# Optimization experiments

Hardware: AMD Instinct MI355X
Metric: run time of the kernel (lower is better)

The kernel has to match this reference:

```python
import jax, jax.numpy as jnp
import numpy as np
import math

B, L, DV = 8, 2048, 512
FACTOR = 5
SAMPLE_K = min(FACTOR * int(np.ceil(np.log(L))), L)  # 40
N_TOP = min(FACTOR * int(np.ceil(np.log(L))), L)     # 40


def setup_inputs() -> dict:
    key = jax.random.key(0)
    k1, k2, k3, k4, k5 = jax.random.split(key, 5)
    x = jax.random.normal(k1, (B, L, DV), dtype=jnp.float32)
    Wq = jax.random.normal(k2, (DV, DV), dtype=jnp.float32) * (1.0 / math.sqrt(DV))
    Wk = jax.random.normal(k3, (DV, DV), dtype=jnp.float32) * (1.0 / math.sqrt(DV))
    Wv = jax.random.normal(k4, (DV, DV), dtype=jnp.float32) * (1.0 / math.sqrt(DV))
    index_sample = jax.random.randint(k5, (L, SAMPLE_K), 0, L, dtype=jnp.int32)
    return {"x": x, "Wq": Wq, "Wk": Wk, "Wv": Wv, "index_sample": index_sample}


def reference(x, Wq, Wk, Wv, index_sample):
    # Projections (torch Linear, no bias): y = x @ W.T
    Q = x @ Wq.T  # [B, L, D]
    K = x @ Wk.T  # [B, L, D]
    V = x @ Wv.T  # [B, L, D]
    b, L_Q, D = Q.shape
    L_K = K.shape[1]

    # _prob_QK: sample keys per query, score sparsity measure M
    K_sample = K[:, index_sample, :]                       # [B, L_Q, sample_k, D]
    QK_sample = jnp.einsum('bld,blsd->bls', Q, K_sample)   # [B, L_Q, sample_k]
    M = QK_sample.max(axis=-1) - QK_sample.sum(axis=-1) / L_K  # [B, L_Q]
    _, M_top = jax.lax.top_k(M, N_TOP)                     # [B, n_top]

    Q_reduce = jnp.take_along_axis(Q, M_top[:, :, None], axis=1)  # [B, n_top, D]
    scores = jnp.einsum('bud,bkd->buk', Q_reduce, K)       # [B, n_top, L_K]
    scores = scores * (1.0 / math.sqrt(D))

    # mask_flag=False -> initial context is mean of V broadcast over queries
    attn = jax.nn.softmax(scores, axis=-1)
    context = jnp.broadcast_to(V.mean(axis=1, keepdims=True), (b, L_Q, D))
    upd = attn @ V                                         # [B, n_top, D]
    context = context.at[jnp.arange(b)[:, None], M_top].set(upd)
    return context
```

## Files before the change

kernel.cpp:

```cpp
#include <hip/hip_runtime.h>
#include <hip/hip_bf16.h>
#include <math.h>

#define BATCH 8
#define LSEQ 2048
#define DIM 512
#define SK 40
#define NTOP 40

typedef __attribute__((ext_vector_type(8))) short bf16x8;
typedef __attribute__((ext_vector_type(4))) float f32x4;

__device__ inline void split1(float f, ushort& h, ushort& l) {
    __hip_bfloat16 bh = __float2bfloat16(f);
    float r = f - __bfloat162float(bh);
    __hip_bfloat16 bl = __float2bfloat16(r);
    h = *reinterpret_cast<ushort*>(&bh);
    l = *reinterpret_cast<ushort*>(&bl);
}

__global__ __launch_bounds__(256) void convert_all(
    const float* __restrict__ x,
    const float* __restrict__ w0, const float* __restrict__ w1, const float* __restrict__ w2,
    ushort* __restrict__ xh, ushort* __restrict__ xl,
    ushort* __restrict__ wh, ushort* __restrict__ wl)
{
    const int bx = blockIdx.x;
    const float* src;
    ushort *dh, *dl;
    int i;
    if (bx < 8192) {
        i = (bx * 256 + (int)threadIdx.x) * 4;
        src = x; dh = xh; dl = xl;
    } else {
        const int j = bx - 8192;
        const int z = j >> 8;
        src = (z == 0) ? w0 : (z == 1) ? w1 : w2;
        dh = wh + (size_t)z * DIM * DIM;
        dl = wl + (size_t)z * DIM * DIM;
        i = ((j & 255) * 256 + (int)threadIdx.x) * 4;
    }
    float4 v = *reinterpret_cast<const float4*>(src + i);
    ushort4 h, l;
    split1(v.x, h.x, l.x); split1(v.y, h.y, l.y);
    split1(v.z, h.z, l.z); split1(v.w, h.w, l.w);
    *reinterpret_cast<ushort4*>(dh + i) = h;
    *reinterpret_cast<ushort4*>(dl + i) = l;
}

__device__ inline void load_lds16(const void* g, void* l) {
    __builtin_amdgcn_global_load_lds(
        (const __attribute__((address_space(1))) void*)g,
        (__attribute__((address_space(3))) void*)l, 16, 0, 0);
}

__global__ __launch_bounds__(256) void gemm_mfma(
    const ushort* __restrict__ xh, const ushort* __restrict__ xl,
    const ushort* __restrict__ whAll, const ushort* __restrict__ wlAll,
    float* __restrict__ Q, float* __restrict__ K, float* __restrict__ V)
{
    const ushort* Wh = whAll + (size_t)blockIdx.z * DIM * DIM;
    const ushort* Wl = wlAll + (size_t)blockIdx.z * DIM * DIM;
    float* C = (blockIdx.z == 0) ? Q : (blockIdx.z == 1) ? K : V;

    __shared__ ushort Ah[128 * 32], Al[128 * 32], Bh[128 * 32], Bl[128 * 32];

    const int tid  = threadIdx.x;
    const int lane = tid & 63;
    const int w    = tid >> 6;
    const int row0 = blockIdx.x * 128;
    const int col0 = blockIdx.y * 128;
    const int wr = w >> 1, wc = w & 1;

    const int rA  = w * 16 + (lane >> 2);
    const int sh_ = (lane & 3) ^ ((rA >> 1) & 3);
    const size_t aoff = (size_t)(row0 + rA) * DIM + sh_ * 8;
    const size_t boff = (size_t)(col0 + rA) * DIM + sh_ * 8;

    f32x4 acc[4][4];
    #pragma unroll
    for (int i = 0; i < 4; ++i)
        #pragma unroll
        for (int j = 0; j < 4; ++j)
            acc[i][j] = (f32x4){0.f, 0.f, 0.f, 0.f};

    const int rbA = wr * 64 + (lane & 15);
    const int rbB = wc * 64 + (lane & 15);
    const int kh  = lane >> 4;

    for (int k0 = 0; k0 < DIM; k0 += 32) {
        load_lds16(xh + aoff + k0,            &Ah[w * 512]);
        load_lds16(xh + aoff + 64 * DIM + k0, &Ah[2048 + w * 512]);
        load_lds16(xl + aoff + k0,            &Al[w * 512]);
        load_lds16(xl + aoff + 64 * DIM + k0, &Al[2048 + w * 512]);
        load_lds16(Wh + boff + k0,            &Bh[w * 512]);
        load_lds16(Wh + boff + 64 * DIM + k0, &Bh[2048 + w * 512]);
        load_lds16(Wl + boff + k0,            &Bl[w * 512]);
        load_lds16(Wl + boff + 64 * DIM + k0, &Bl[2048 + w * 512]);
        __syncthreads();

        bf16x8 fah[4], fal[4], fbh[4], fbl[4];
        #pragma unroll
        for (int mf = 0; mf < 4; ++mf) {
            const int r = rbA + mf * 16;
            const int off = r * 32 + (kh ^ ((r >> 1) & 3)) * 8;
            fah[mf] = *reinterpret_cast<const bf16x8*>(&Ah[off]);
            fal[mf] = *reinterpret_cast<const bf16x8*>(&Al[off]);
        }
        #pragma unroll
        for (int nf = 0; nf < 4; ++nf) {
            const int r = rbB + nf * 16;
            const int off = r * 32 + (kh ^ ((r >> 1) & 3)) * 8;
            fbh[nf] = *reinterpret_cast<const bf16x8*>(&Bh[off]);
            fbl[nf] = *reinterpret_cast<const bf16x8*>(&Bl[off]);
        }
        #pragma unroll
        for (int mf = 0; mf < 4; ++mf)
            #pragma unroll
            for (int nf = 0; nf < 4; ++nf) {
                acc[mf][nf] = __builtin_amdgcn_mfma_f32_16x16x32_bf16(fah[mf], fbh[nf], acc[mf][nf], 0, 0, 0);
                acc[mf][nf] = __builtin_amdgcn_mfma_f32_16x16x32_bf16(fal[mf], fbh[nf], acc[mf][nf], 0, 0, 0);
                acc[mf][nf] = __builtin_amdgcn_mfma_f32_16x16x32_bf16(fah[mf], fbl[nf], acc[mf][nf], 0, 0, 0);
            }
        __syncthreads();
    }

    #pragma unroll
    for (int mf = 0; mf < 4; ++mf)
        #pragma unroll
        for (int nf = 0; nf < 4; ++nf) {
            float* cp = C + (size_t)(row0 + wr * 64 + mf * 16 + (lane >> 4) * 4) * DIM
                          + col0 + wc * 64 + nf * 16 + (lane & 15);
            #pragma unroll
            for (int j = 0; j < 4; ++j)
                cp[(size_t)j * DIM] = acc[mf][nf][j];
        }
}

#define BM 64
#define BN 64
#define BKD 32
__global__ __launch_bounds__(256) void gemm_qkv(
    const float* __restrict__ x,
    const float* __restrict__ Wq, const float* __restrict__ Wk, const float* __restrict__ Wv,
    float* __restrict__ Q, float* __restrict__ K, float* __restrict__ V)
{
    const float* W;
    float* C;
    if (blockIdx.z == 0)      { W = Wq; C = Q; }
    else if (blockIdx.z == 1) { W = Wk; C = K; }
    else                      { W = Wv; C = V; }

    __shared__ float As[BKD][BM];
    __shared__ float Bs[BKD][BN];

    const int tid  = threadIdx.x;
    const int row0 = blockIdx.x * BM;
    const int col0 = blockIdx.y * BN;
    const int ty   = tid >> 4;
    const int tx   = tid & 15;
    const int lrow = tid >> 3;
    const int lkq  = tid & 7;

    float acc[4][4] = {};
    for (int k0 = 0; k0 < DIM; k0 += BKD) {
        #pragma unroll
        for (int h = 0; h < 2; ++h) {
            const int arow = lrow + h * 32;
            float4 va = *reinterpret_cast<const float4*>(&x[(size_t)(row0 + arow) * DIM + k0 + lkq * 4]);
            As[lkq * 4 + 0][arow] = va.x; As[lkq * 4 + 1][arow] = va.y;
            As[lkq * 4 + 2][arow] = va.z; As[lkq * 4 + 3][arow] = va.w;
            float4 vb = *reinterpret_cast<const float4*>(&W[(size_t)(col0 + arow) * DIM + k0 + lkq * 4]);
            Bs[lkq * 4 + 0][arow] = vb.x; Bs[lkq * 4 + 1][arow] = vb.y;
            Bs[lkq * 4 + 2][arow] = vb.z; Bs[lkq * 4 + 3][arow] = vb.w;
        }
        __syncthreads();
        #pragma unroll
        for (int kk = 0; kk < BKD; ++kk) {
            float4 a4 = *reinterpret_cast<const float4*>(&As[kk][ty * 4]);
            float4 b4 = *reinterpret_cast<const float4*>(&Bs[kk][tx * 4]);
            float af[4] = {a4.x, a4.y, a4.z, a4.w};
            float bf[4] = {b4.x, b4.y, b4.z, b4.w};
            #pragma unroll
            for (int i = 0; i < 4; ++i)
                #pragma unroll
                for (int j = 0; j < 4; ++j)
                    acc[i][j] += af[i] * bf[j];
        }
        __syncthreads();
    }
    #pragma unroll
    for (int i = 0; i < 4; ++i) {
        float4 o = make_float4(acc[i][0], acc[i][1], acc[i][2], acc[i][3]);
        *reinterpret_cast<float4*>(&C[(size_t)(row0 + ty * 4 + i) * DIM + col0 + tx * 4]) = o;
    }
}

__global__ __launch_bounds__(256) void compute_m(
    const float* __restrict__ Q, const float* __restrict__ K,
    const int* __restrict__ smp, float* __restrict__ M)
{
    const int wv   = threadIdx.x >> 6;
    const int lane = threadIdx.x & 63;
    const int b    = blockIdx.x & 7;
    const int l    = (blockIdx.x >> 3) * 4 + wv;

    const float* qr = Q + ((size_t)b * LSEQ + l) * DIM;
    float4 q0 = *reinterpret_cast<const float4*>(&qr[lane * 8]);
    float4 q1 = *reinterpret_cast<const float4*>(&qr[lane * 8 + 4]);

    const int* sp = smp + l * SK;
    const float* Kb = K + (size_t)b * LSEQ * DIM;

    float mx = -1e30f, sm = 0.0f;
    for (int s = 0; s < SK; s += 4) {
        int4 id = *reinterpret_cast<const int4*>(sp + s);
        const float* r0 = Kb + (size_t)id.x * DIM + lane * 8;
        const float* r1 = Kb + (size_t)id.y * DIM + lane * 8;
        const float* r2 = Kb + (size_t)id.z * DIM + lane * 8;
        const float* r3 = Kb + (size_t)id.w * DIM + lane * 8;
        float4 a0 = *reinterpret_cast<const float4*>(r0);
        float4 a1 = *reinterpret_cast<const float4*>(r0 + 4);
        float4 b0 = *reinterpret_cast<const float4*>(r1);
        float4 b1 = *reinterpret_cast<const float4*>(r1 + 4);
        float4 c0 = *reinterpret_cast<const float4*>(r2);
        float4 c1 = *reinterpret_cast<const float4*>(r2 + 4);
        float4 d0 = *reinterpret_cast<const float4*>(r3);
        float4 d1 = *reinterpret_cast<const float4*>(r3 + 4);

        float p0 = q0.x*a0.x + q0.y*a0.y + q0.z*a0.z + q0.w*a0.w
                 + q1.x*a1.x + q1.y*a1.y + q1.z*a1.z + q1.w*a1.w;
        float p1 = q0.x*b0.x + q0.y*b0.y + q0.z*b0.z + q0.w*b0.w
                 + q1.x*b1.x + q1.y*b1.y + q1.z*b1.z + q1.w*b1.w;
        float p2 = q0.x*c0.x + q0.y*c0.y + q0.z*c0.z + q0.w*c0.w
                 + q1.x*c1.x + q1.y*c1.y + q1.z*c1.z + q1.w*c1.w;
        float p3 = q0.x*d0.x + q0.y*d0.y + q0.z*d0.z + q0.w*d0.w
                 + q1.x*d1.x + q1.y*d1.y + q1.z*d1.z + q1.w*d1.w;
        #pragma unroll
        for (int o = 32; o; o >>= 1) {
            p0 += __shfl_xor(p0, o, 64);
            p1 += __shfl_xor(p1, o, 64);
            p2 += __shfl_xor(p2, o, 64);
            p3 += __shfl_xor(p3, o, 64);
        }
        mx = fmaxf(mx, fmaxf(fmaxf(p0, p1), fmaxf(p2, p3)));
        sm += (p0 + p1) + (p2 + p3);
    }
    if (lane == 0) M[(size_t)b * LSEQ + l] = mx - sm * (1.0f / LSEQ);
}

__global__ __launch_bounds__(1024) void topk_kernel(
    const float* __restrict__ M, int* __restrict__ topidx)
{
    const int b = blockIdx.x;
    __shared__ float vals[LSEQ];
    __shared__ float wv[16];
    __shared__ int   wi[16];
    const int tid  = threadIdx.x;
    const int lane = tid & 63;
    const int wave = tid >> 6;

    vals[tid]        = M[b * LSEQ + tid];
    vals[tid + 1024] = M[b * LSEQ + tid + 1024];
    __syncthreads();

    for (int t = 0; t < NTOP; ++t) {
        float v0 = vals[tid], v1 = vals[tid + 1024];
        float bv; int bi;
        if (v0 >= v1) { bv = v0; bi = tid; } else { bv = v1; bi = tid + 1024; }
        #pragma unroll
        for (int o = 32; o; o >>= 1) {
            float ov = __shfl_xor(bv, o, 64);
            int   oi = __shfl_xor(bi, o, 64);
            if (ov > bv || (ov == bv && oi < bi)) { bv = ov; bi = oi; }
        }
        if (lane == 0) { wv[wave] = bv; wi[wave] = bi; }
        __syncthreads();
        if (wave == 0) {
            float fv = (lane < 16) ? wv[lane] : -1e30f;
            int   fi = (lane < 16) ? wi[lane] : 0x7fffffff;
            #pragma unroll
            for (int o = 8; o; o >>= 1) {
                float ov = __shfl_xor(fv, o, 64);
                int   oi = __shfl_xor(fi, o, 64);
                if (ov > fv || (ov == fv && oi < fi)) { fv = ov; fi = oi; }
            }
            if (lane == 0) {
                topidx[b * NTOP + t] = fi;
                vals[fi] = -1e30f;
            }
        }
        __syncthreads();
    }
}

__global__ __launch_bounds__(256) void vmean_partial(
    const float* __restrict__ V, float* __restrict__ P)
{
    const int b = blockIdx.x & 7, c = blockIdx.x >> 3;
    const int tid = threadIdx.x;
    #pragma unroll
    for (int dd = 0; dd < 2; ++dd) {
        const int d = tid + dd * 256;
        const float* vp = V + ((size_t)b * LSEQ + c * 128) * DIM + d;
        float s = 0.0f;
        for (int r = 0; r < 128; ++r) s += vp[(size_t)r * DIM];
        P[(size_t)(b * 16 + c) * DIM + d] = s;
    }
}

__global__ __launch_bounds__(256) void vmean_reduce(
    const float* __restrict__ P, float* __restrict__ vmean)
{
    const int b = blockIdx.x;
    const int tid = threadIdx.x;
    #pragma unroll
    for (int dd = 0; dd < 2; ++dd) {
        const int d = tid + dd * 256;
        float s = 0.0f;
        #pragma unroll
        for (int c = 0; c < 16; ++c) s += P[(size_t)(b * 16 + c) * DIM + d];
        vmean[b * DIM + d] = s * (1.0f / LSEQ);
    }
}

__global__ __launch_bounds__(256) void fill_out(
    const float4* __restrict__ vmean4, float4* __restrict__ out4)
{
    const int f = blockIdx.x * 256 + threadIdx.x;
    const int d4 = f & 127;
    const int b  = f >> 18;
    out4[f] = vmean4[b * 128 + d4];
}

__global__ __launch_bounds__(256) void scores_kernel(
    const float* __restrict__ Q, const float* __restrict__ K,
    const int* __restrict__ topidx, float* __restrict__ S)
{
    const int b  = blockIdx.x & 7;
    const int lc = blockIdx.x >> 3;
    __shared__ float Qs[40 * 132];
    __shared__ float Ks[64 * 132];
    __shared__ int tix[NTOP];
    const int tid = threadIdx.x;
    const int lt  = tid & 31;
    const int ug  = tid >> 5;
    float acc[2][5] = {};

    if (tid < NTOP) tix[tid] = topidx[b * NTOP + tid];
    __syncthreads();

    for (int d0 = 0; d0 < DIM; d0 += 128) {
        for (int j = tid; j < 1280; j += 256) {
            const int u = j >> 5, d4 = j & 31;
            *reinterpret_cast<float4*>(&Qs[u * 132 + d4 * 4]) =
                *reinterpret_cast<const float4*>(&Q[((size_t)b * LSEQ + tix[u]) * DIM + d0 + d4 * 4]);
        }
        for (int j = tid; j < 2048; j += 256) {
            const int l = j >> 5, d4 = j & 31;
            *reinterpret_cast<float4*>(&Ks[l * 132 + d4 * 4]) =
                *reinterpret_cast<const float4*>(&K[((size_t)b * LSEQ + lc * 64 + l) * DIM + d0 + d4 * 4]);
        }
        __syncthreads();
        for (int d4 = 0; d4 < 32; ++d4) {
            float4 ka = *reinterpret_cast<const float4*>(&Ks[lt * 132 + d4 * 4]);
            float4 kb = *reinterpret_cast<const float4*>(&Ks[(lt + 32) * 132 + d4 * 4]);
            #pragma unroll
            for (int i = 0; i < 5; ++i) {
                float4 q = *reinterpret_cast<const float4*>(&Qs[(ug + i * 8) * 132 + d4 * 4]);
                acc[0][i] += q.x * ka.x + q.y * ka.y + q.z * ka.z + q.w * ka.w;
                acc[1][i] += q.x * kb.x + q.y * kb.y + q.z * kb.z + q.w * kb.w;
            }
        }
        __syncthreads();
    }
    const float scale = 0.044194173824159216f;
    #pragma unroll
    for (int i = 0; i < 5; ++i) {
        const int u = ug + i * 8;
        S[((size_t)(b * NTOP + u)) * LSEQ + lc * 64 + lt]      = acc[0][i] * scale;
        S[((size_t)(b * NTOP + u)) * LSEQ + lc * 64 + lt + 32] = acc[1][i] * scale;
    }
}

__global__ __launch_bounds__(256) void softmax_kernel(
    const float* __restrict__ S, float* __restrict__ Pt)
{
    const int row = blockIdx.x;
    const int b = row / NTOP, u = row % NTOP;
    __shared__ float red[4];
    const int tid  = threadIdx.x;
    const int lane = tid & 63;
    const int wave = tid >> 6;
    const float* sr = S + (size_t)row * LSEQ;

    float v[8];
    float mx = -1e30f;
    #pragma unroll
    for (int j = 0; j < 8; ++j) { v[j] = sr[tid + j * 256]; mx = fmaxf(mx, v[j]); }
    #pragma unroll
    for (int o = 32; o; o >>= 1) mx = fmaxf(mx, __shfl_xor(mx, o, 64));
    if (lane == 0) red[wave] = mx;
    __syncthreads();
    mx = fmaxf(fmaxf(red[0], red[1]), fmaxf(red[2], red[3]));
    __syncthreads();

    float s = 0.0f;
    #pragma unroll
    for (int j = 0; j < 8; ++j) { v[j] = __expf(v[j] - mx); s += v[j]; }
    #pragma unroll
    for (int o = 32; o; o >>= 1) s += __shfl_xor(s, o, 64);
    if (lane == 0) red[wave] = s;
    __syncthreads();
    const float rec = 1.0f / (red[0] + red[1] + red[2] + red[3]);

    #pragma unroll
    for (int j = 0; j < 8; ++j)
        Pt[((size_t)b * LSEQ + tid + j * 256) * NTOP + u] = v[j] * rec;
}

__global__ __launch_bounds__(512) void pv_partial(
    const float* __restrict__ Pt, const float* __restrict__ V, float* __restrict__ Ppart)
{
    const int b  = blockIdx.x & 7;
    const int lc = blockIdx.x >> 3;
    const int d  = threadIdx.x;
    float part[NTOP] = {};
    for (int l = 0; l < 128; ++l) {
        const float v = V[((size_t)b * LSEQ + lc * 128 + l) * DIM + d];
        const float* ps = Pt + ((size_t)b * LSEQ + lc * 128 + l) * NTOP;
        #pragma unroll
        for (int u = 0; u < NTOP; ++u) part[u] = fmaf(ps[u], v, part[u]);
    }
    #pragma unroll
    for (int u = 0; u < NTOP; ++u)
        Ppart[(((size_t)(b * 16 + lc)) * NTOP + u) * DIM + d] = part[u];
}

__global__ __launch_bounds__(512) void pv_reduce(
    const float* __restrict__ Ppart, const int* __restrict__ topidx, float* __restrict__ out)
{
    const int row = blockIdx.x;
    const int b = row / NTOP, u = row % NTOP;
    const int d = threadIdx.x;
    float s = 0.0f;
    #pragma unroll
    for (int lc = 0; lc < 16; ++lc)
        s += Ppart[(((size_t)(b * 16 + lc)) * NTOP + u) * DIM + d];
    out[((size_t)b * LSEQ + topidx[row]) * DIM + d] = s;
}

__global__ __launch_bounds__(256) void att_kernel(
    const float* __restrict__ Q, const float* __restrict__ K, const float* __restrict__ V,
    const int* __restrict__ topidx, float* __restrict__ out)
{
    const int b = blockIdx.x / NTOP;
    const int u = blockIdx.x % NTOP;
    const int l0 = topidx[b * NTOP + u];

    __shared__ float p[LSEQ];
    __shared__ float redm[4];
    __shared__ float reds[4];

    const int tid  = threadIdx.x;
    const int lane = tid & 63;
    const int wave = tid >> 6;

    const float* qr = Q + ((size_t)b * LSEQ + l0) * DIM;
    float4 q0 = *reinterpret_cast<const float4*>(&qr[lane * 8]);
    float4 q1 = *reinterpret_cast<const float4*>(&qr[lane * 8 + 4]);
    const float scale = 0.044194173824159216f;

    for (int it = 0; it < 512; ++it) {
        const int l = wave * 512 + it;
        const float* kr = K + ((size_t)b * LSEQ + l) * DIM;
        float4 k0 = *reinterpret_cast<const float4*>(&kr[lane * 8]);
        float4 k1 = *reinterpret_cast<const float4*>(&kr[lane * 8 + 4]);
        float d = q0.x * k0.x + q0.y * k0.y + q0.z * k0.z + q0.w * k0.w
                + q1.x * k1.x + q1.y * k1.y + q1.z * k1.z + q1.w * k1.w;
        #pragma unroll
        for (int o = 32; o; o >>= 1) d += __shfl_xor(d, o, 64);
        if (lane == 0) p[l] = d * scale;
    }
    __syncthreads();

    float mx = -1e30f;
    for (int i = tid; i < LSEQ; i += 256) mx = fmaxf(mx, p[i]);
    #pragma unroll
    for (int o = 32; o; o >>= 1) mx = fmaxf(mx, __shfl_xor(mx, o, 64));
    if (lane == 0) redm[wave] = mx;
    __syncthreads();
    mx = fmaxf(fmaxf(redm[0], redm[1]), fmaxf(redm[2], redm[3]));

    float s = 0.0f;
    for (int i = tid; i < LSEQ; i += 256) {
        float e = __expf(p[i] - mx);
        s += e;
        p[i] = e;
    }
    #pragma unroll
    for (int o = 32; o; o >>= 1) s += __shfl_xor(s, o, 64);
    if (lane == 0) reds[wave] = s;
    __syncthreads();
    const float rec = 1.0f / (reds[0] + reds[1] + reds[2] + reds[3]);

    float s0 = 0.0f, s1 = 0.0f;
    const float* vp = V + (size_t)b * LSEQ * DIM;
    for (int l = 0; l < LSEQ; ++l) {
        const float w = p[l];
        s0 += w * vp[(size_t)l * DIM + tid];
        s1 += w * vp[(size_t)l * DIM + tid + 256];
    }
    float* orow = out + ((size_t)b * LSEQ + l0) * DIM;
    orow[tid]       = s0 * rec;
    orow[tid + 256] = s1 * rec;
}

extern "C" void kernel_launch(void* const* d_in, const int* in_sizes, int n_in,
                              void* d_out, int out_size, void* d_ws, size_t ws_size,
                              hipStream_t stream)
{
    const float* x   = (const float*)d_in[0];
    const float* Wq  = (const float*)d_in[1];
    const float* Wk  = (const float*)d_in[2];
    const float* Wv  = (const float*)d_in[3];
    const int*   smp = (const int*)d_in[4];
    float* out = (float*)d_out;

    const size_t NQKV = (size_t)BATCH * LSEQ * DIM;
    float* ws = (float*)d_ws;

    float* Q     = ws;
    float* K     = Q + NQKV;
    float* V     = K + NQKV;
    float* Mb    = V + NQKV;
    float* vmP   = Mb + BATCH * LSEQ;
    float* vmean = vmP + BATCH * 16 * DIM;
    float* S     = vmean + BATCH * DIM;
    float* Pt    = S + (size_t)BATCH * NTOP * LSEQ;
    float* Qsel  = Pt + (size_t)BATCH * NTOP * LSEQ;
    float* Ppart = Qsel + (size_t)BATCH * NTOP * DIM;
    int*   topidx = (int*)(Ppart + (size_t)BATCH * 16 * NTOP * DIM);
    ushort* xh = (ushort*)(topidx + BATCH * NTOP);
    ushort* xl = xh + NQKV;
    ushort* wh = xl + NQKV;
    ushort* wl = wh + (size_t)3 * DIM * DIM;
    const size_t need_fast = (size_t)((char*)(wl + (size_t)3 * DIM * DIM) - (char*)d_ws);
    const size_t need_mid  = (size_t)((char*)(topidx + BATCH * NTOP) - (char*)d_ws);

    const bool fast = ws_size >= need_fast;
    const bool mid  = ws_size >= need_mid;

    if (mid) {
        if (fast) {
            convert_all<<<8960, 256, 0, stream>>>(x, Wq, Wk, Wv, xh, xl, wh, wl);
            gemm_mfma<<<dim3(BATCH * LSEQ / 128, DIM / 128, 3), 256, 0, stream>>>(
                xh, xl, wh, wl, Q, K, V);
        } else {
            gemm_qkv<<<dim3(BATCH * LSEQ / BM, DIM / BN, 3), 256, 0, stream>>>(
                x, Wq, Wk, Wv, Q, K, V);
        }
        compute_m<<<4096, 256, 0, stream>>>(Q, K, smp, Mb);
        topk_kernel<<<BATCH, 1024, 0, stream>>>(Mb, topidx);
        vmean_partial<<<BATCH * 16, 256, 0, stream>>>(V, vmP);
        vmean_reduce<<<BATCH, 256, 0, stream>>>(vmP, vmean);
        fill_out<<<(BATCH * LSEQ * DIM / 4) / 256, 256, 0, stream>>>(
            (const float4*)vmean, (float4*)out);
        scores_kernel<<<256, 256, 0, stream>>>(Q, K, topidx, S);
        softmax_kernel<<<BATCH * NTOP, 256, 0, stream>>>(S, Pt);
        pv_partial<<<128, 512, 0, stream>>>(Pt, V, Ppart);
        pv_reduce<<<BATCH * NTOP, 512, 0, stream>>>(Ppart, topidx, out);
    } else {
        float* Qf = ws;
        float* Kf = Qf + NQKV;
        float* Vf = Kf + NQKV;
        float* Mf = Vf + NQKV;
        int*   ti = (int*)(Mf + (size_t)BATCH * LSEQ);
        float* Pf = (float*)(ti + BATCH * NTOP);
        float* vm = Pf + (size_t)BATCH * 16 * DIM;

        gemm_qkv<<<dim3(BATCH * LSEQ / BM, DIM / BN, 3), 256, 0, stream>>>(
            x, Wq, Wk, Wv, Qf, Kf, Vf);
        compute_m<<<4096, 256, 0, stream>>>(Qf, Kf, smp, Mf);
        topk_kernel<<<BATCH, 1024, 0, stream>>>(Mf, ti);
        vmean_partial<<<BATCH * 16, 256, 0, stream>>>(Vf, Pf);
        vmean_reduce<<<BATCH, 256, 0, stream>>>(Pf, vm);
        fill_out<<<(BATCH * LSEQ * DIM / 4) / 256, 256, 0, stream>>>(
            (const float4*)vm, (float4*)out);
        att_kernel<<<BATCH * NTOP, 256, 0, stream>>>(Qf, Kf, Vf, ti, out);
    }
}
```

Baseline: 321.4 us.

## Rewrite QKV split-bf16 GEMM as 256x128 tile, 8-wave, double-buffered pipeline

Replaces the 128x128, 4-wave GEMM with a 256x128, 8-wave kernel. The three hi/lo bf16 product terms are folded into a single 24-step K loop (3 terms x 8 chunks of 64), with double-buffered LDS staging via global_load_lds, explicit vmcnt waits and barriers, and s_setprio around the MFMA bursts. Blocks are remapped with an XCD-aware swizzle so neighbouring tiles share L2, and each block's columns stay within one of Q/K/V. The aim is to overlap global loads with MFMA work and get more reuse per tile, at the cost of more LDS (96 KB) and hand-tuned waitcnt logic that is fragile.

```diff
diff --git a/kernel.cpp b/kernel.cpp
--- a/kernel.cpp
+++ b/kernel.cpp
@@ -54,28 +54,59 @@
         (__attribute__((address_space(3))) void*)l, 16, 0, 0);
 }
 
-__global__ __launch_bounds__(256) void gemm_mfma(
+__global__ __launch_bounds__(512) void gemm8(
     const ushort* __restrict__ xh, const ushort* __restrict__ xl,
     const ushort* __restrict__ whAll, const ushort* __restrict__ wlAll,
     float* __restrict__ Q, float* __restrict__ K, float* __restrict__ V)
 {
-    const ushort* Wh = whAll + (size_t)blockIdx.z * DIM * DIM;
-    const ushort* Wl = wlAll + (size_t)blockIdx.z * DIM * DIM;
-    float* C = (blockIdx.z == 0) ? Q : (blockIdx.z == 1) ? K : V;
-
-    __shared__ ushort Ah[128 * 32], Al[128 * 32], Bh[128 * 32], Bl[128 * 32];
+    __shared__ ushort SA[32768];
+    __shared__ ushort SB[16384];
 
     const int tid  = threadIdx.x;
     const int lane = tid & 63;
     const int w    = tid >> 6;
-    const int row0 = blockIdx.x * 128;
-    const int col0 = blockIdx.y * 128;
-    const int wr = w >> 1, wc = w & 1;
-
-    const int rA  = w * 16 + (lane >> 2);
-    const int sh_ = (lane & 3) ^ ((rA >> 1) & 3);
-    const size_t aoff = (size_t)(row0 + rA) * DIM + sh_ * 8;
-    const size_t boff = (size_t)(col0 + rA) * DIM + sh_ * 8;
+    const int wr   = w >> 1;
+    const int wcn  = w & 1;
+
+    const int wg = ((int)blockIdx.x & 7) * 96 + ((int)blockIdx.x >> 3);
+    const int mb = wg / 12, nb = wg % 12;
+    const int z  = nb >> 2;
+    float* C = (z == 0) ? Q : (z == 1) ? K : V;
+    const int row0  = mb * 256;
+    const int wrow0 = (nb & 3) * 128;
+    const ushort* whb = whAll + (size_t)z * (DIM * DIM);
+    const ushort* wlb = wlAll + (size_t)z * (DIM * DIM);
+
+    int rA[2], dA[2]; size_t sA[2];
+    #pragma unroll
+    for (int i = 0; i < 2; ++i) {
+        const int g = i * 512 + tid;
+        const int row = g >> 2, sl = g & 3;
+        const int ss = sl ^ ((row >> 1) & 3);
+        rA[i] = row;
+        dA[i] = (g & ~63) * 8;
+        sA[i] = (size_t)(row0 + row) * DIM + ss * 8;
+    }
+    int dB; size_t sB;
+    {
+        const int g = tid;
+        const int row = g >> 2, sl = g & 3;
+        const int ss = sl ^ ((row >> 1) & 3);
+        dB = (g & ~63) * 8;
+        sB = (size_t)(wrow0 + row) * DIM + ss * 8;
+    }
+
+    int aoff[4], boff[4];
+    #pragma unroll
+    for (int mf = 0; mf < 4; ++mf) {
+        const int row = wr * 64 + mf * 16 + (lane & 15);
+        aoff[mf] = row * 32 + (((lane >> 4) ^ ((row >> 1) & 3)) * 8);
+    }
+    #pragma unroll
+    for (int nf = 0; nf < 4; ++nf) {
+        const int row = wcn * 64 + nf * 16 + (lane & 15);
+        boff[nf] = row * 32 + (((lane >> 4) ^ ((row >> 1) & 3)) * 8);
+    }
 
     f32x4 acc[4][4];
     #pragma unroll
@@ -84,53 +115,83 @@
         for (int j = 0; j < 4; ++j)
             acc[i][j] = (f32x4){0.f, 0.f, 0.f, 0.f};
 
-    const int rbA = wr * 64 + (lane & 15);
-    const int rbB = wc * 64 + (lane & 15);
-    const int kh  = lane >> 4;
-
-    for (int k0 = 0; k0 < DIM; k0 += 32) {
-        load_lds16(xh + aoff + k0,            &Ah[w * 512]);
-        load_lds16(xh + aoff + 64 * DIM + k0, &Ah[2048 + w * 512]);
-        load_lds16(xl + aoff + k0,            &Al[w * 512]);
-        load_lds16(xl + aoff + 64 * DIM + k0, &Al[2048 + w * 512]);
-        load_lds16(Wh + boff + k0,            &Bh[w * 512]);
-        load_lds16(Wh + boff + 64 * DIM + k0, &Bh[2048 + w * 512]);
-        load_lds16(Wl + boff + k0,            &Bl[w * 512]);
-        load_lds16(Wl + boff + 64 * DIM + k0, &Bl[2048 + w * 512]);
-        __syncthreads();
-
-        bf16x8 fah[4], fal[4], fbh[4], fbl[4];
-        #pragma unroll
-        for (int mf = 0; mf < 4; ++mf) {
-            const int r = rbA + mf * 16;
-            const int off = r * 32 + (kh ^ ((r >> 1) & 3)) * 8;
-            fah[mf] = *reinterpret_cast<const bf16x8*>(&Ah[off]);
-            fal[mf] = *reinterpret_cast<const bf16x8*>(&Al[off]);
-        }
-        #pragma unroll
-        for (int nf = 0; nf < 4; ++nf) {
-            const int r = rbB + nf * 16;
-            const int off = r * 32 + (kh ^ ((r >> 1) & 3)) * 8;
-            fbh[nf] = *reinterpret_cast<const bf16x8*>(&Bh[off]);
-            fbl[nf] = *reinterpret_cast<const bf16x8*>(&Bl[off]);
-        }
-        #pragma unroll
-        for (int mf = 0; mf < 4; ++mf)
-            #pragma unroll
-            for (int nf = 0; nf < 4; ++nf) {
-                acc[mf][nf] = __builtin_amdgcn_mfma_f32_16x16x32_bf16(fah[mf], fbh[nf], acc[mf][nf], 0, 0, 0);
-                acc[mf][nf] = __builtin_amdgcn_mfma_f32_16x16x32_bf16(fal[mf], fbh[nf], acc[mf][nf], 0, 0, 0);
-                acc[mf][nf] = __builtin_amdgcn_mfma_f32_16x16x32_bf16(fah[mf], fbl[nf], acc[mf][nf], 0, 0, 0);
-            }
-        __syncthreads();
-    }
+#define STAGE_CHUNK(t_, ks_, cb_)                                              \
+    {                                                                          \
+        const int tt_ = (t_) >> 3;                                             \
+        const int ksrc_ = (((t_) & 7) << 6) + ((ks_) << 5);                    \
+        const ushort* ap_ = (tt_ == 1) ? xl : xh;                              \
+        const ushort* bp_ = (tt_ == 2) ? wlb : whb;                            \
+        const int ab_ = ((cb_) * 2 + (ks_)) * 8192;                            \
+        const int bb_ = ((cb_) * 2 + (ks_)) * 4096;                            \
+        load_lds16(ap_ + sA[0] + ksrc_, &SA[ab_ + dA[0]]);                     \
+        load_lds16(ap_ + sA[1] + ksrc_, &SA[ab_ + dA[1]]);                     \
+        load_lds16(bp_ + sB + ksrc_,    &SB[bb_ + dB]);                        \
+    }
+
+    STAGE_CHUNK(0, 0, 0)
+    STAGE_CHUNK(0, 1, 0)
+    STAGE_CHUNK(1, 0, 1)
+    asm volatile("s_waitcnt vmcnt(6)" ::: "memory");
+    asm volatile("s_barrier" ::: "memory");
+
+    #pragma unroll 2
+    for (int t = 0; t < 24; ++t) {
+        const int cb = t & 1;
+        {
+            bf16x8 af[4], bf_[4];
+            const int ab = (cb * 2 + 0) * 8192;
+            const int bb = (cb * 2 + 0) * 4096;
+            #pragma unroll
+            for (int mf = 0; mf < 4; ++mf)
+                af[mf] = *reinterpret_cast<const bf16x8*>(&SA[ab + aoff[mf]]);
+            #pragma unroll
+            for (int nf = 0; nf < 4; ++nf)
+                bf_[nf] = *reinterpret_cast<const bf16x8*>(&SB[bb + boff[nf]]);
+            if (t + 1 < 24) STAGE_CHUNK(t + 1, 1, cb ^ 1)
+            asm volatile("s_waitcnt vmcnt(6)" ::: "memory");
+            asm volatile("s_barrier" ::: "memory");
+            __builtin_amdgcn_s_setprio(1);
+            #pragma unroll
+            for (int mf = 0; mf < 4; ++mf)
+                #pragma unroll
+                for (int nf = 0; nf < 4; ++nf)
+                    acc[mf][nf] = __builtin_amdgcn_mfma_f32_16x16x32_bf16(
+                        af[mf], bf_[nf], acc[mf][nf], 0, 0, 0);
+            __builtin_amdgcn_s_setprio(0);
+            asm volatile("s_barrier" ::: "memory");
+        }
+        {
+            bf16x8 af[4], bf_[4];
+            const int ab = (cb * 2 + 1) * 8192;
+            const int bb = (cb * 2 + 1) * 4096;
+            #pragma unroll
+            for (int mf = 0; mf < 4; ++mf)
+                af[mf] = *reinterpret_cast<const bf16x8*>(&SA[ab + aoff[mf]]);
+            #pragma unroll
+            for (int nf = 0; nf < 4; ++nf)
+                bf_[nf] = *reinterpret_cast<const bf16x8*>(&SB[bb + boff[nf]]);
+            if (t + 2 < 24) STAGE_CHUNK(t + 2, 0, cb)
+            asm volatile("s_waitcnt vmcnt(6)" ::: "memory");
+            asm volatile("s_barrier" ::: "memory");
+            __builtin_amdgcn_s_setprio(1);
+            #pragma unroll
+            for (int mf = 0; mf < 4; ++mf)
+                #pragma unroll
+                for (int nf = 0; nf < 4; ++nf)
+                    acc[mf][nf] = __builtin_amdgcn_mfma_f32_16x16x32_bf16(
+                        af[mf], bf_[nf], acc[mf][nf], 0, 0, 0);
+            __builtin_amdgcn_s_setprio(0);
+            asm volatile("s_barrier" ::: "memory");
+        }
+    }
+#undef STAGE_CHUNK
 
     #pragma unroll
     for (int mf = 0; mf < 4; ++mf)
         #pragma unroll
         for (int nf = 0; nf < 4; ++nf) {
             float* cp = C + (size_t)(row0 + wr * 64 + mf * 16 + (lane >> 4) * 4) * DIM
-                          + col0 + wc * 64 + nf * 16 + (lane & 15);
+                          + wrow0 + wcn * 64 + nf * 16 + (lane & 15);
             #pragma unroll
             for (int j = 0; j < 4; ++j)
                 cp[(size_t)j * DIM] = acc[mf][nf][j];
@@ -554,8 +615,7 @@
     if (mid) {
         if (fast) {
             convert_all<<<8960, 256, 0, stream>>>(x, Wq, Wk, Wv, xh, xl, wh, wl);
-            gemm_mfma<<<dim3(BATCH * LSEQ / 128, DIM / 128, 3), 256, 0, stream>>>(
-                xh, xl, wh, wl, Q, K, V);
+            gemm8<<<768, 512, 0, stream>>>(xh, xl, wh, wl, Q, K, V);
         } else {
             gemm_qkv<<<dim3(BATCH * LSEQ / BM, DIM / BN, 3), 256, 0, stream>>>(
                 x, Wq, Wk, Wv, Q, K, V);
```

After: 336.7 us. 4.7% more time.

## Fuse sparsity-score with V-mean partials and top-k with V-mean reduce

Applied to the files above, without the earlier changes.

Merges compute_m and vmean_partial into one launch whose blocks are split by block index, and likewise merges top-k selection with the V-mean reduction. Two kernel launches are removed and the independent V-mean work runs alongside the M computation and top-k. The M loop now issues 8 gathered K rows per iteration with 512-thread blocks, exposing more memory parallelism. Top-k uses 512 threads scanning 4 values each. The trade-off is a longer serial per-thread scan in the top-k loop and higher register use in the M loop.

```diff
diff --git a/kernel.cpp b/kernel.cpp
--- a/kernel.cpp
+++ b/kernel.cpp
@@ -196,112 +196,52 @@
     }
 }
 
-__global__ __launch_bounds__(256) void compute_m(
+__global__ __launch_bounds__(512) void m_and_vp(
     const float* __restrict__ Q, const float* __restrict__ K,
-    const int* __restrict__ smp, float* __restrict__ M)
-{
-    const int wv   = threadIdx.x >> 6;
-    const int lane = threadIdx.x & 63;
-    const int b    = blockIdx.x & 7;
-    const int l    = (blockIdx.x >> 3) * 4 + wv;
-
-    const float* qr = Q + ((size_t)b * LSEQ + l) * DIM;
-    float4 q0 = *reinterpret_cast<const float4*>(&qr[lane * 8]);
-    float4 q1 = *reinterpret_cast<const float4*>(&qr[lane * 8 + 4]);
-
-    const int* sp = smp + l * SK;
-    const float* Kb = K + (size_t)b * LSEQ * DIM;
-
-    float mx = -1e30f, sm = 0.0f;
-    for (int s = 0; s < SK; s += 4) {
-        int4 id = *reinterpret_cast<const int4*>(sp + s);
-        const float* r0 = Kb + (size_t)id.x * DIM + lane * 8;
-        const float* r1 = Kb + (size_t)id.y * DIM + lane * 8;
-        const float* r2 = Kb + (size_t)id.z * DIM + lane * 8;
-        const float* r3 = Kb + (size_t)id.w * DIM + lane * 8;
-        float4 a0 = *reinterpret_cast<const float4*>(r0);
-        float4 a1 = *reinterpret_cast<const float4*>(r0 + 4);
-        float4 b0 = *reinterpret_cast<const float4*>(r1);
-        float4 b1 = *reinterpret_cast<const float4*>(r1 + 4);
-        float4 c0 = *reinterpret_cast<const float4*>(r2);
-        float4 c1 = *reinterpret_cast<const float4*>(r2 + 4);
-        float4 d0 = *reinterpret_cast<const float4*>(r3);
-        float4 d1 = *reinterpret_cast<const float4*>(r3 + 4);
-
-        float p0 = q0.x*a0.x + q0.y*a0.y + q0.z*a0.z + q0.w*a0.w
-                 + q1.x*a1.x + q1.y*a1.y + q1.z*a1.z + q1.w*a1.w;
-        float p1 = q0.x*b0.x + q0.y*b0.y + q0.z*b0.z + q0.w*b0.w
-                 + q1.x*b1.x + q1.y*b1.y + q1.z*b1.z + q1.w*b1.w;
-        float p2 = q0.x*c0.x + q0.y*c0.y + q0.z*c0.z + q0.w*c0.w
-                 + q1.x*c1.x + q1.y*c1.y + q1.z*c1.z + q1.w*c1.w;
-        float p3 = q0.x*d0.x + q0.y*d0.y + q0.z*d0.z + q0.w*d0.w
-                 + q1.x*d1.x + q1.y*d1.y + q1.z*d1.z + q1.w*d1.w;
-        #pragma unroll
-        for (int o = 32; o; o >>= 1) {
-            p0 += __shfl_xor(p0, o, 64);
-            p1 += __shfl_xor(p1, o, 64);
-            p2 += __shfl_xor(p2, o, 64);
-            p3 += __shfl_xor(p3, o, 64);
-        }
-        mx = fmaxf(mx, fmaxf(fmaxf(p0, p1), fmaxf(p2, p3)));
-        sm += (p0 + p1) + (p2 + p3);
-    }
-    if (lane == 0) M[(size_t)b * LSEQ + l] = mx - sm * (1.0f / LSEQ);
-}
-
-__global__ __launch_bounds__(1024) void topk_kernel(
-    const float* __restrict__ M, int* __restrict__ topidx)
-{
-    const int b = blockIdx.x;
-    __shared__ float vals[LSEQ];
-    __shared__ float wv[16];
-    __shared__ int   wi[16];
-    const int tid  = threadIdx.x;
-    const int lane = tid & 63;
-    const int wave = tid >> 6;
-
-    vals[tid]        = M[b * LSEQ + tid];
-    vals[tid + 1024] = M[b * LSEQ + tid + 1024];
-    __syncthreads();
-
-    for (int t = 0; t < NTOP; ++t) {
-        float v0 = vals[tid], v1 = vals[tid + 1024];
-        float bv; int bi;
-        if (v0 >= v1) { bv = v0; bi = tid; } else { bv = v1; bi = tid + 1024; }
-        #pragma unroll
-        for (int o = 32; o; o >>= 1) {
-            float ov = __shfl_xor(bv, o, 64);
-            int   oi = __shfl_xor(bi, o, 64);
-            if (ov > bv || (ov == bv && oi < bi)) { bv = ov; bi = oi; }
-        }
-        if (lane == 0) { wv[wave] = bv; wi[wave] = bi; }
-        __syncthreads();
-        if (wave == 0) {
-            float fv = (lane < 16) ? wv[lane] : -1e30f;
-            int   fi = (lane < 16) ? wi[lane] : 0x7fffffff;
-            #pragma unroll
-            for (int o = 8; o; o >>= 1) {
-                float ov = __shfl_xor(fv, o, 64);
-                int   oi = __shfl_xor(fi, o, 64);
-                if (ov > fv || (ov == fv && oi < fi)) { fv = ov; fi = oi; }
-            }
-            if (lane == 0) {
-                topidx[b * NTOP + t] = fi;
-                vals[fi] = -1e30f;
-            }
-        }
-        __syncthreads();
-    }
-}
-
-__global__ __launch_bounds__(256) void vmean_partial(
-    const float* __restrict__ V, float* __restrict__ P)
-{
-    const int b = blockIdx.x & 7, c = blockIdx.x >> 3;
-    const int tid = threadIdx.x;
-    #pragma unroll
-    for (int dd = 0; dd < 2; ++dd) {
-        const int d = tid + dd * 256;
+    const float* __restrict__ V, const int* __restrict__ smp,
+    float* __restrict__ M, float* __restrict__ P)
+{
+    const int bid = blockIdx.x;
+    if (bid < 2048) {
+        const int wv   = threadIdx.x >> 6;
+        const int lane = threadIdx.x & 63;
+        const int b    = bid & 7;
+        const int l    = (bid >> 3) * 8 + wv;
+
+        const float* qr = Q + ((size_t)b * LSEQ + l) * DIM;
+        float4 q0 = *reinterpret_cast<const float4*>(&qr[lane * 8]);
+        float4 q1 = *reinterpret_cast<const float4*>(&qr[lane * 8 + 4]);
+
+        const int* sp = smp + l * SK;
+        const float* Kb = K + (size_t)b * LSEQ * DIM;
+
+        float mx = -1e30f, sm = 0.0f;
+        for (int s = 0; s < SK; s += 8) {
+            int4 i0 = *reinterpret_cast<const int4*>(sp + s);
+            int4 i1 = *reinterpret_cast<const int4*>(sp + s + 4);
+            const int id[8] = {i0.x, i0.y, i0.z, i0.w, i1.x, i1.y, i1.z, i1.w};
+            float p[8];
+            #pragma unroll
+            for (int j = 0; j < 8; ++j) {
+                const float* r = Kb + (size_t)id[j] * DIM + lane * 8;
+                float4 u0 = *reinterpret_cast<const float4*>(r);
+                float4 u1 = *reinterpret_cast<const float4*>(r + 4);
+                p[j] = q0.x*u0.x + q0.y*u0.y + q0.z*u0.z + q0.w*u0.w
+                     + q1.x*u1.x + q1.y*u1.y + q1.z*u1.z + q1.w*u1.w;
+            }
+            #pragma unroll
+            for (int o = 32; o; o >>= 1) {
+                #pragma unroll
+                for (int j = 0; j < 8; ++j) p[j] += __shfl_xor(p[j], o, 64);
+            }
+            #pragma unroll
+            for (int j = 0; j < 8; ++j) { mx = fmaxf(mx, p[j]); sm += p[j]; }
+        }
+        if (lane == 0) M[(size_t)b * LSEQ + l] = mx - sm * (1.0f / LSEQ);
+    } else {
+        const int j = bid - 2048;
+        const int b = j & 7, c = j >> 3;
+        const int d = threadIdx.x;
         const float* vp = V + ((size_t)b * LSEQ + c * 128) * DIM + d;
         float s = 0.0f;
         for (int r = 0; r < 128; ++r) s += vp[(size_t)r * DIM];
@@ -309,14 +249,60 @@
     }
 }
 
-__global__ __launch_bounds__(256) void vmean_reduce(
-    const float* __restrict__ P, float* __restrict__ vmean)
-{
-    const int b = blockIdx.x;
-    const int tid = threadIdx.x;
-    #pragma unroll
-    for (int dd = 0; dd < 2; ++dd) {
-        const int d = tid + dd * 256;
+__global__ __launch_bounds__(512) void topk_vr(
+    const float* __restrict__ M, const float* __restrict__ P,
+    int* __restrict__ topidx, float* __restrict__ vmean)
+{
+    __shared__ float vals[LSEQ];
+    __shared__ float wvv[8];
+    __shared__ int   wii[8];
+
+    if (blockIdx.x < 8) {
+        const int b = blockIdx.x;
+        const int tid  = threadIdx.x;
+        const int lane = tid & 63;
+        const int wave = tid >> 6;
+
+        #pragma unroll
+        for (int q = 0; q < 4; ++q) vals[tid + q * 512] = M[b * LSEQ + tid + q * 512];
+        __syncthreads();
+
+        for (int t = 0; t < NTOP; ++t) {
+            float bv = -1e30f;
+            int   bi = 0x7fffffff;
+            #pragma unroll
+            for (int q = 0; q < 4; ++q) {
+                const int ii = tid + q * 512;
+                const float v = vals[ii];
+                if (v > bv) { bv = v; bi = ii; }
+            }
+            #pragma unroll
+            for (int o = 32; o; o >>= 1) {
+                float ov = __shfl_xor(bv, o, 64);
+                int   oi = __shfl_xor(bi, o, 64);
+                if (ov > bv || (ov == bv && oi < bi)) { bv = ov; bi = oi; }
+            }
+            if (lane == 0) { wvv[wave] = bv; wii[wave] = bi; }
+            __syncthreads();
+            if (wave == 0) {
+                float fv = (lane < 8) ? wvv[lane] : -1e30f;
+                int   fi = (lane < 8) ? wii[lane] : 0x7fffffff;
+                #pragma unroll
+                for (int o = 4; o; o >>= 1) {
+                    float ov = __shfl_xor(fv, o, 64);
+                    int   oi = __shfl_xor(fi, o, 64);
+                    if (ov > fv || (ov == fv && oi < fi)) { fv = ov; fi = oi; }
+                }
+                if (lane == 0) {
+                    topidx[b * NTOP + t] = fi;
+                    vals[fi] = -1e30f;
+                }
+            }
+            __syncthreads();
+        }
+    } else {
+        const int b = blockIdx.x - 8;
+        const int d = threadIdx.x;
         float s = 0.0f;
         #pragma unroll
         for (int c = 0; c < 16; ++c) s += P[(size_t)(b * 16 + c) * DIM + d];
@@ -560,10 +546,8 @@
             gemm_qkv<<<dim3(BATCH * LSEQ / BM, DIM / BN, 3), 256, 0, stream>>>(
                 x, Wq, Wk, Wv, Q, K, V);
         }
-        compute_m<<<4096, 256, 0, stream>>>(Q, K, smp, Mb);
-        topk_kernel<<<BATCH, 1024, 0, stream>>>(Mb, topidx);
-        vmean_partial<<<BATCH * 16, 256, 0, stream>>>(V, vmP);
-        vmean_reduce<<<BATCH, 256, 0, stream>>>(vmP, vmean);
+        m_and_vp<<<2176, 512, 0, stream>>>(Q, K, V, smp, Mb, vmP);
+        topk_vr<<<16, 512, 0, stream>>>(Mb, vmP, topidx, vmean);
         fill_out<<<(BATCH * LSEQ * DIM / 4) / 256, 256, 0, stream>>>(
             (const float4*)vmean, (float4*)out);
         scores_kernel<<<256, 256, 0, stream>>>(Q, K, topidx, S);
@@ -581,10 +565,8 @@
 
         gemm_qkv<<<dim3(BATCH * LSEQ / BM, DIM / BN, 3), 256, 0, stream>>>(
             x, Wq, Wk, Wv, Qf, Kf, Vf);
-        compute_m<<<4096, 256, 0, stream>>>(Qf, Kf, smp, Mf);
-        topk_kernel<<<BATCH, 1024, 0, stream>>>(Mf, ti);
-        vmean_partial<<<BATCH * 16, 256, 0, stream>>>(Vf, Pf);
-        vmean_reduce<<<BATCH, 256, 0, stream>>>(Pf, vm);
+        m_and_vp<<<2176, 512, 0, stream>>>(Qf, Kf, Vf, smp, Mf, Pf);
+        topk_vr<<<16, 512, 0, stream>>>(Mf, Pf, ti, vm);
         fill_out<<<(BATCH * LSEQ * DIM / 4) / 256, 256, 0, stream>>>(
             (const float4*)vm, (float4*)out);
         att_kernel<<<BATCH * NTOP, 256, 0, stream>>>(Qf, Kf, Vf, ti, out);
```

Measured after the change: 306.6 us. -4.6%, faster.
